# Performance work log

Hardware: AMD Instinct MI355X
Metric: run time of the kernel (lower is better)

Reference implementation:

```python
import jax, jax.numpy as jnp
import numpy as np

N = 100000   # nodes
E = 1600000  # edges (before self loops)
IN, HID, HEADS, OUT = 128, 32, 2, 32


def setup_inputs() -> dict:
    key = jax.random.key(0)
    ks = jax.random.split(key, 10)
    def glorot(k, shape, fan_in):
        return jax.random.normal(k, shape, dtype=jnp.float32) / np.sqrt(fan_in)
    return {
        "x": jax.random.normal(ks[0], (N, IN), dtype=jnp.float32),
        "edge_index": jax.random.randint(ks[1], (2, E), 0, N, dtype=jnp.int32),
        "W1": glorot(ks[2], (IN, HEADS * HID), IN),
        "a_src1": glorot(ks[3], (HEADS, HID), HID),
        "a_dst1": glorot(ks[4], (HEADS, HID), HID),
        "b1": jnp.zeros((HEADS * HID,), dtype=jnp.float32),
        "W2": glorot(ks[5], (HEADS * HID, OUT), HEADS * HID),
        "a_src2": glorot(ks[6], (1, OUT), OUT),
        "a_dst2": glorot(ks[7], (1, OUT), OUT),
        "b2": jnp.zeros((OUT,), dtype=jnp.float32),
    }


def gat_conv(x, W, a_src, a_dst, b, src, dst, n):
    """PyG-style GATConv: shared linear, edge softmax over incoming edges, sum aggregate."""
    H, C = a_src.shape
    xl = (x @ W).reshape(n, H, C)                       # [N, H, C]
    asn = jnp.einsum('nhc,hc->nh', xl, a_src)            # per-node source score
    adn = jnp.einsum('nhc,hc->nh', xl, a_dst)            # per-node dest score
    e = jax.nn.leaky_relu(asn[src] + adn[dst], 0.2)      # [E', H]
    m = jax.ops.segment_max(e, dst, num_segments=n)      # stable softmax per dest
    m = jnp.where(jnp.isfinite(m), m, 0.0)
    ex = jnp.exp(e - m[dst])
    denom = jax.ops.segment_sum(ex, dst, num_segments=n)
    alpha = ex / (denom[dst] + 1e-16)                    # [E', H]
    out = jax.ops.segment_sum(xl[src] * alpha[:, :, None], dst, num_segments=n)
    return out.reshape(n, H * C) + b


def reference(x, edge_index, W1, a_src1, a_dst1, b1, W2, a_src2, a_dst2, b2):
    n = x.shape[0]
    loop = jnp.arange(n, dtype=edge_index.dtype)         # add self loops (PyG default)
    src = jnp.concatenate([edge_index[0], loop])
    dst = jnp.concatenate([edge_index[1], loop])
    h = jax.nn.relu(gat_conv(x, W1, a_src1, a_dst1, b1, src, dst, n))
    # F.dropout(p=0.5) is identity in eval mode
    return gat_conv(h, W2, a_src2, a_dst2, b2, src, dst, n)
```

## Files before the change

### kernel.cpp

```cpp
#include <hip/hip_runtime.h>
#include <hip/hip_fp16.h>


#define BS 256
#define PCHUNK 8192
#define CAPB 5632
#define GPAD 16

typedef _Float16 half8 __attribute__((ext_vector_type(8)));
typedef float f32x4 __attribute__((ext_vector_type(4)));

__global__ __launch_bounds__(BS) void k_init(int* __restrict__ gcursor, int nbuk) {
    for (int i = threadIdx.x; i < nbuk; i += BS) gcursor[i * GPAD] = i * CAPB;
}

__global__ __launch_bounds__(BS) void k_pg1(const int* __restrict__ ei, int E, int n,
                                            int* __restrict__ gcursor, int* __restrict__ ppair,
                                            const float* __restrict__ x, const float* __restrict__ W,
                                            const float* __restrict__ asrc, const float* __restrict__ adst,
                                            __half* __restrict__ xl, float* __restrict__ sc, int gC) {
    __shared__ _Float16 smem[8192];
    int tid = threadIdx.x;
    if ((int)blockIdx.x < gC) {
        int* cnt  = (int*)smem;
        int* gpos = cnt + 512;
        int* lcur = cnt + 1024;
        cnt[tid] = 0; cnt[tid + 256] = 0;
        lcur[tid] = 0; lcur[tid + 256] = 0;
        __syncthreads();
        const int* dstp = ei + E;
        int base = blockIdx.x * PCHUNK;
        bool full = (base + PCHUNK <= E);
        if (full) {
            const int4* dv = (const int4*)(dstp + base) + tid * 8;
#pragma unroll
            for (int k = 0; k < 8; k++) {
                int4 d4 = dv[k];
                atomicAdd(&cnt[d4.x >> 8], 1);
                atomicAdd(&cnt[d4.y >> 8], 1);
                atomicAdd(&cnt[d4.z >> 8], 1);
                atomicAdd(&cnt[d4.w >> 8], 1);
            }
        } else {
            for (int i = tid; base + i < E; i += BS)
                atomicAdd(&cnt[dstp[base + i] >> 8], 1);
        }
        __syncthreads();
        for (int b = tid; b < 512; b += BS) {
            int c = cnt[b];
            if (c > 0) gpos[b] = atomicAdd(&gcursor[b * GPAD], c);
        }
        __syncthreads();
        if (full) {
            const int4* sv = (const int4*)(ei + base) + tid * 8;
            const int4* dv = (const int4*)(dstp + base) + tid * 8;
#pragma unroll 2
            for (int k = 0; k < 8; k++) {
                int4 s4 = sv[k];
                int4 d4 = dv[k];
                int d, s, b, r;
                d = d4.x; s = s4.x; b = d >> 8; r = atomicAdd(&lcur[b], 1);
                ppair[gpos[b] + r] = ((d & 255) << 17) | s;
                d = d4.y; s = s4.y; b = d >> 8; r = atomicAdd(&lcur[b], 1);
                ppair[gpos[b] + r] = ((d & 255) << 17) | s;
                d = d4.z; s = s4.z; b = d >> 8; r = atomicAdd(&lcur[b], 1);
                ppair[gpos[b] + r] = ((d & 255) << 17) | s;
                d = d4.w; s = s4.w; b = d >> 8; r = atomicAdd(&lcur[b], 1);
                ppair[gpos[b] + r] = ((d & 255) << 17) | s;
            }
        } else {
            for (int i = tid; base + i < E; i += BS) {
                int s = ei[base + i], d = dstp[base + i];
                int b = d >> 8;
                int r = atomicAdd(&lcur[b], 1);
                ppair[gpos[b] + r] = ((d & 255) << 17) | s;
            }
        }
        return;
    }
    _Float16* wf = smem;
#pragma unroll
    for (int v = 0; v < 8; v++) {
        int w = (v * 256 + tid) * 4;
        float4 ww = *(const float4*)(W + w);
        int k = w >> 6, c0 = w & 63;
        int kt = k >> 5, j = k & 7, lnh = (k >> 3) & 3;
        int nt = c0 >> 4;
        int f = kt * 4 + nt;
        int bidx = (f * 64 + lnh * 16 + (c0 & 15)) * 8 + j;
        wf[bidx]      = (_Float16)ww.x;
        wf[bidx + 8]  = (_Float16)ww.y;
        wf[bidx + 16] = (_Float16)ww.z;
        wf[bidx + 24] = (_Float16)ww.w;
    }
    __syncthreads();
    int wave = tid >> 6, lane = tid & 63;
    int nb = ((blockIdx.x - gC) * 4 + wave) * 16;
    int m = lane & 15, q = lane >> 4;
    int node_m = nb + m; if (node_m >= n) node_m = n - 1;
    half8 bf[4][4];
#pragma unroll
    for (int f = 0; f < 16; f++)
        bf[f >> 2][f & 3] = *(half8*)&wf[(f * 64 + lane) * 8];
    f32x4 acc[4] = {f32x4{0,0,0,0}, f32x4{0,0,0,0}, f32x4{0,0,0,0}, f32x4{0,0,0,0}};
#pragma unroll
    for (int kt = 0; kt < 4; kt++) {
        const float* xp = x + (size_t)node_m * 128 + kt * 32 + q * 8;
        float4 xa = *(const float4*)xp;
        float4 xb = *(const float4*)(xp + 4);
        half8 a;
        a[0] = (_Float16)xa.x; a[1] = (_Float16)xa.y; a[2] = (_Float16)xa.z; a[3] = (_Float16)xa.w;
        a[4] = (_Float16)xb.x; a[5] = (_Float16)xb.y; a[6] = (_Float16)xb.z; a[7] = (_Float16)xb.w;
#pragma unroll
        for (int nt = 0; nt < 4; nt++)
            acc[nt] = __builtin_amdgcn_mfma_f32_16x16x32_f16(a, bf[kt][nt], acc[nt], 0, 0, 0);
    }
    int c = lane & 15;
    float a_s[4], a_d[4];
#pragma unroll
    for (int nt = 0; nt < 4; nt++) { a_s[nt] = asrc[nt * 16 + c]; a_d[nt] = adst[nt * 16 + c]; }
#pragma unroll
    for (int r = 0; r < 4; r++) {
        int node = nb + q * 4 + r;
        bool ok = node < n;
        float v0 = acc[0][r], v1 = acc[1][r], v2 = acc[2][r], v3 = acc[3][r];
        float as0 = v0 * a_s[0] + v1 * a_s[1];
        float as1 = v2 * a_s[2] + v3 * a_s[3];
        float ad0 = v0 * a_d[0] + v1 * a_d[1];
        float ad1 = v2 * a_d[2] + v3 * a_d[3];
#pragma unroll
        for (int off = 1; off < 16; off <<= 1) {
            as0 += __shfl_xor(as0, off); as1 += __shfl_xor(as1, off);
            ad0 += __shfl_xor(ad0, off); ad1 += __shfl_xor(ad1, off);
        }
        if (ok) {
            __half* row = xl + (size_t)node * 64;
            row[c]      = __float2half(v0);
            row[16 + c] = __float2half(v1);
            row[32 + c] = __float2half(v2);
            row[48 + c] = __float2half(v3);
            if (c == 0) ((float4*)sc)[node] = make_float4(as0, as1, ad0, ad1);
        }
    }
}

__global__ __launch_bounds__(BS) void k_bucket(const int* __restrict__ ppair,
                                               const int* __restrict__ gcursor, int n,
                                               int* __restrict__ col,
                                               int* __restrict__ row_ptr, int* __restrict__ row_end) {
    __shared__ int ldeg[256];
    __shared__ int lscan[256];
    __shared__ int lcur[256];
    __shared__ int lcol[CAPB];
    int b = blockIdx.x;
    int t = threadIdx.x;
    int lo = b << 8;
    int hi = lo + 256; if (hi > n) hi = n;
    int W = hi - lo;
    int base = b * CAPB;
    int cnt = gcursor[b * GPAD] - base;
    if (cnt > CAPB) cnt = CAPB;
    ldeg[t] = 0;
    __syncthreads();
    for (int i = t; i < cnt; i += BS)
        atomicAdd(&ldeg[ppair[base + i] >> 17], 1);
    __syncthreads();
    lscan[t] = ldeg[t];
    __syncthreads();
    for (int off = 1; off < 256; off <<= 1) {
        int a = (t >= off) ? lscan[t - off] : 0;
        __syncthreads();
        lscan[t] += a;
        __syncthreads();
    }
    {
        int e0 = lscan[t] - ldeg[t];
        lcur[t] = e0;
        if (t < W) { row_ptr[lo + t] = base + e0; row_end[lo + t] = base + e0 + ldeg[t]; }
    }
    __syncthreads();
    for (int i = t; i < cnt; i += BS) {
        int p = ppair[base + i];
        int r = atomicAdd(&lcur[p >> 17], 1);
        if (r < CAPB) lcol[r] = p & 131071;
    }
    __syncthreads();
    for (int i = t; i < cnt; i += BS) col[base + i] = lcol[i];
}

__global__ __launch_bounds__(BS) void k_ag1g2(const int* __restrict__ row_ptr, const int* __restrict__ row_end,
                                              const int* __restrict__ col, const __half* __restrict__ xl,
                                              const float* __restrict__ sc, const float* __restrict__ asrc,
                                              const float* __restrict__ b1,
                                              const float* __restrict__ W2,
                                              const float* __restrict__ as2, const float* __restrict__ ad2,
                                              __half* __restrict__ xl2, float* __restrict__ sc2, int n) {
    __shared__ _Float16 hsh[32 * 72];
    __shared__ _Float16 wf2[2048];
    int tid = threadIdx.x;
#pragma unroll
    for (int v = 0; v < 2; v++) {
        int w = (v * 256 + tid) * 4;
        float4 ww = *(const float4*)(W2 + w);
        int k = w >> 5, c0 = w & 31;
        int kt = k >> 5, j = k & 7, lnh = (k >> 3) & 3;
        int nt = c0 >> 4;
        int f = kt * 2 + nt;
        int bidx = (f * 64 + lnh * 16 + (c0 & 15)) * 8 + j;
        wf2[bidx]      = (_Float16)ww.x;
        wf2[bidx + 8]  = (_Float16)ww.y;
        wf2[bidx + 16] = (_Float16)ww.z;
        wf2[bidx + 24] = (_Float16)ww.w;
    }
    int node_local = tid >> 3;
    int node = blockIdx.x * 32 + node_local;
    int tc = tid & 7;
    int lane = tid & 63;
    int tb = lane & 56;
    bool alive = node < n;
    int nodeC = alive ? node : n - 1;
    float4 acA = ((const float4*)asrc)[tc * 2];
    float4 acB = ((const float4*)asrc)[tc * 2 + 1];
    int s0 = row_ptr[nodeC], e1 = row_end[nodeC];
    float4 sn = ((const float4*)sc)[nodeC];
    bool hh0 = tc < 4;
    float adn = hh0 ? sn.z : sn.w;
    float es0 = sn.x + sn.z; es0 = fmaxf(es0, 0.2f * es0);
    float es1 = sn.y + sn.w; es1 = fmaxf(es1, 0.2f * es1);
    float xs = __expf(hh0 ? es0 : es1);
    uint4 rawS = *(const uint4*)(xl + (size_t)nodeC * 64 + tc * 8);
    __half2 sh0 = *(__half2*)&rawS.x, sh1 = *(__half2*)&rawS.y;
    __half2 sh2 = *(__half2*)&rawS.z, sh3 = *(__half2*)&rawS.w;
    float acc0 = xs * __low2float(sh0), acc1 = xs * __high2float(sh0);
    float acc2 = xs * __low2float(sh1), acc3 = xs * __high2float(sh1);
    float acc4 = xs * __low2float(sh2), acc5 = xs * __high2float(sh2);
    float acc6 = xs * __low2float(sh3), acc7 = xs * __high2float(sh3);
    float den = xs;
    int deg = e1 - s0;
    int mx = deg;
    mx = max(mx, __shfl_xor(mx, 8));
    mx = max(mx, __shfl_xor(mx, 16));
    mx = max(mx, __shfl_xor(mx, 32));
    int nch = (mx + 7) >> 3;
    for (int ci = 0; ci < nch; ci++) {
        int pos = s0 + ci * 8;
        int m = e1 - pos; m = m < 0 ? 0 : (m > 8 ? 8 : m);
        int srcv = (tc < m) ? col[pos + tc] : 0;
#pragma unroll
        for (int kb = 0; kb < 8; kb += 4) {
            int rem = m - kb;
            if (rem > 0) {
                int nv = rem < 4 ? rem : 4;
                uint4 rr[4];
#pragma unroll
                for (int k = 0; k < 4; k++) {
                    if (k < nv) {
                        int sE = __shfl(srcv, tb + kb + k);
                        rr[k] = *(const uint4*)(xl + (size_t)sE * 64 + tc * 8);
                    }
                }
#pragma unroll
                for (int k = 0; k < 4; k++) {
                    if (k < nv) {
                        __half2 q0 = *(__half2*)&rr[k].x, q1 = *(__half2*)&rr[k].y;
                        __half2 q2 = *(__half2*)&rr[k].z, q3 = *(__half2*)&rr[k].w;
                        float f0 = __low2float(q0), f1 = __high2float(q0);
                        float f2 = __low2float(q1), f3 = __high2float(q1);
                        float f4 = __low2float(q2), f5 = __high2float(q2);
                        float f6 = __low2float(q3), f7 = __high2float(q3);
                        float dA = f0 * acA.x + f1 * acA.y + f2 * acA.z + f3 * acA.w;
                        float dB = f4 * acB.x + f5 * acB.y + f6 * acB.z + f7 * acB.w;
                        float dot = dA + dB;
                        dot += __shfl_xor(dot, 1);
                        dot += __shfl_xor(dot, 2);
                        float e = dot + adn; e = fmaxf(e, 0.2f * e);
                        float w = __expf(e);
                        acc0 = fmaf(w, f0, acc0); acc1 = fmaf(w, f1, acc1);
                        acc2 = fmaf(w, f2, acc2); acc3 = fmaf(w, f3, acc3);
                        acc4 = fmaf(w, f4, acc4); acc5 = fmaf(w, f5, acc5);
                        acc6 = fmaf(w, f6, acc6); acc7 = fmaf(w, f7, acc7);
                        den += w;
                    }
                }
            }
        }
    }
    float dinv = 1.f / (den + 1e-16f);
    {
        float4 bvA = ((const float4*)b1)[tc * 2];
        float4 bvB = ((const float4*)b1)[tc * 2 + 1];
        __half2 p0 = __floats2half2_rn(fmaxf(fmaf(acc0, dinv, bvA.x), 0.f),
                                       fmaxf(fmaf(acc1, dinv, bvA.y), 0.f));
        __half2 p1 = __floats2half2_rn(fmaxf(fmaf(acc2, dinv, bvA.z), 0.f),
                                       fmaxf(fmaf(acc3, dinv, bvA.w), 0.f));
        __half2 p2 = __floats2half2_rn(fmaxf(fmaf(acc4, dinv, bvB.x), 0.f),
                                       fmaxf(fmaf(acc5, dinv, bvB.y), 0.f));
        __half2 p3 = __floats2half2_rn(fmaxf(fmaf(acc6, dinv, bvB.z), 0.f),
                                       fmaxf(fmaf(acc7, dinv, bvB.w), 0.f));
        uint4 o;
        o.x = *(unsigned int*)&p0; o.y = *(unsigned int*)&p1;
        o.z = *(unsigned int*)&p2; o.w = *(unsigned int*)&p3;
        *(uint4*)&hsh[node_local * 72 + tc * 8] = o;
    }
    __syncthreads();
    int wave = tid >> 6;
    if (wave < 2) {
        int m2 = lane & 15, q2 = lane >> 4;
        int nl = wave * 16 + m2;
        half8 bf[2][2];
#pragma unroll
        for (int f = 0; f < 4; f++)
            bf[f >> 1][f & 1] = *(half8*)&wf2[(f * 64 + lane) * 8];
        f32x4 acc2g[2] = {f32x4{0,0,0,0}, f32x4{0,0,0,0}};
#pragma unroll
        for (int kt = 0; kt < 2; kt++) {
            half8 a = *(half8*)&hsh[nl * 72 + kt * 32 + q2 * 8];
#pragma unroll
            for (int nt = 0; nt < 2; nt++)
                acc2g[nt] = __builtin_amdgcn_mfma_f32_16x16x32_f16(a, bf[kt][nt], acc2g[nt], 0, 0, 0);
        }
        int c = lane & 15;
        float a_s[2], a_d[2];
#pragma unroll
        for (int nt = 0; nt < 2; nt++) { a_s[nt] = as2[nt * 16 + c]; a_d[nt] = ad2[nt * 16 + c]; }
#pragma unroll
        for (int r = 0; r < 4; r++) {
            int nl_r = wave * 16 + q2 * 4 + r;
            int node_r = blockIdx.x * 32 + nl_r;
            bool ok = node_r < n;
            float v0 = acc2g[0][r], v1 = acc2g[1][r];
            float as = v0 * a_s[0] + v1 * a_s[1];
            float ad = v0 * a_d[0] + v1 * a_d[1];
#pragma unroll
            for (int off = 1; off < 16; off <<= 1) {
                as += __shfl_xor(as, off); ad += __shfl_xor(ad, off);
            }
            if (ok) {
                __half* row = xl2 + (size_t)node_r * 32;
                row[c]      = __float2half(v0);
                row[16 + c] = __float2half(v1);
                if (c == 0) ((float2*)sc2)[node_r] = make_float2(as, ad);
            }
        }
    }
}

__global__ __launch_bounds__(BS) void k_agg2(const int* __restrict__ row_ptr, const int* __restrict__ row_end,
                                             const int* __restrict__ col, const __half* __restrict__ xl,
                                             const float* __restrict__ sc, const float* __restrict__ asrc,
                                             const float* __restrict__ b2,
                                             float* __restrict__ out, int n) {
    int tid = blockIdx.x * BS + threadIdx.x;
    int node = tid >> 2;
    int tc = threadIdx.x & 3;
    int lane = threadIdx.x & 63;
    int tb = lane & 60;
    bool alive = node < n;
    if (!alive) node = n - 1;
    float4 acA = ((const float4*)asrc)[tc * 2];
    float4 acB = ((const float4*)asrc)[tc * 2 + 1];
    int s0 = row_ptr[node], e1 = row_end[node];
    float2 sn = ((const float2*)sc)[node];
    float adn = sn.y;
    float es = sn.x + adn; es = fmaxf(es, 0.2f * es);
    float xs = __expf(es);
    uint4 rawS = *(const uint4*)(xl + (size_t)node * 32 + tc * 8);
    __half2 sh0 = *(__half2*)&rawS.x, sh1 = *(__half2*)&rawS.y;
    __half2 sh2 = *(__half2*)&rawS.z, sh3 = *(__half2*)&rawS.w;
    float acc0 = xs * __low2float(sh0), acc1 = xs * __high2float(sh0);
    float acc2 = xs * __low2float(sh1), acc3 = xs * __high2float(sh1);
    float acc4 = xs * __low2float(sh2), acc5 = xs * __high2float(sh2);
    float acc6 = xs * __low2float(sh3), acc7 = xs * __high2float(sh3);
    float den = xs;
    int deg = e1 - s0;
    int mx = deg;
    mx = max(mx, __shfl_xor(mx, 4));
    mx = max(mx, __shfl_xor(mx, 8));
    mx = max(mx, __shfl_xor(mx, 16));
    mx = max(mx, __shfl_xor(mx, 32));
    int nch = (mx + 3) >> 2;
    for (int ci = 0; ci < nch; ci++) {
        int pos = s0 + ci * 4;
        int m = e1 - pos; m = m < 0 ? 0 : (m > 4 ? 4 : m);
        int srcv = (tc < m) ? col[pos + tc] : 0;
        if (m > 0) {
            uint4 rr[4];
#pragma unroll
            for (int k = 0; k < 4; k++) {
                if (k < m) {
                    int sE = __shfl(srcv, tb + k);
                    rr[k] = *(const uint4*)(xl + (size_t)sE * 32 + tc * 8);
                }
            }
#pragma unroll
            for (int k = 0; k < 4; k++) {
                if (k < m) {
                    __half2 q0 = *(__half2*)&rr[k].x, q1 = *(__half2*)&rr[k].y;
                    __half2 q2 = *(__half2*)&rr[k].z, q3 = *(__half2*)&rr[k].w;
                    float f0 = __low2float(q0), f1 = __high2float(q0);
                    float f2 = __low2float(q1), f3 = __high2float(q1);
                    float f4 = __low2float(q2), f5 = __high2float(q2);
                    float f6 = __low2float(q3), f7 = __high2float(q3);
                    float dA = f0 * acA.x + f1 * acA.y + f2 * acA.z + f3 * acA.w;
                    float dB = f4 * acB.x + f5 * acB.y + f6 * acB.z + f7 * acB.w;
                    float dot = dA + dB;
                    dot += __shfl_xor(dot, 1);
                    dot += __shfl_xor(dot, 2);
                    float e = dot + adn; e = fmaxf(e, 0.2f * e);
                    float w = __expf(e);
                    acc0 = fmaf(w, f0, acc0); acc1 = fmaf(w, f1, acc1);
                    acc2 = fmaf(w, f2, acc2); acc3 = fmaf(w, f3, acc3);
                    acc4 = fmaf(w, f4, acc4); acc5 = fmaf(w, f5, acc5);
                    acc6 = fmaf(w, f6, acc6); acc7 = fmaf(w, f7, acc7);
                    den += w;
                }
            }
        }
    }
    float dinv = 1.f / (den + 1e-16f);
    if (alive) {
        float4 bvA = ((const float4*)b2)[tc * 2];
        float4 bvB = ((const float4*)b2)[tc * 2 + 1];
        float4 oA, oB;
        oA.x = fmaf(acc0, dinv, bvA.x);
        oA.y = fmaf(acc1, dinv, bvA.y);
        oA.z = fmaf(acc2, dinv, bvA.z);
        oA.w = fmaf(acc3, dinv, bvA.w);
        oB.x = fmaf(acc4, dinv, bvB.x);
        oB.y = fmaf(acc5, dinv, bvB.y);
        oB.z = fmaf(acc6, dinv, bvB.z);
        oB.w = fmaf(acc7, dinv, bvB.w);
        float4* orow = (float4*)(out + (size_t)node * 32);
        orow[tc * 2]     = oA;
        orow[tc * 2 + 1] = oB;
    }
}

extern "C" void kernel_launch(void* const* d_in, const int* in_sizes, int n_in,
                              void* d_out, int out_size, void* d_ws, size_t ws_size,
                              hipStream_t stream) {
    const float* x    = (const float*)d_in[0];
    const int*   ei   = (const int*)d_in[1];
    const float* W1   = (const float*)d_in[2];
    const float* as1  = (const float*)d_in[3];
    const float* ad1  = (const float*)d_in[4];
    const float* b1   = (const float*)d_in[5];
    const float* W2   = (const float*)d_in[6];
    const float* as2  = (const float*)d_in[7];
    const float* ad2  = (const float*)d_in[8];
    const float* b2   = (const float*)d_in[9];
    int n = in_sizes[0] / 128;
    int E = in_sizes[1] / 2;
    int NBUK = (n + 255) >> 8;

    char* w = (char*)d_ws;
    auto alloc = [&](size_t bytes) -> char* {
        char* p = w; w += (bytes + 255) / 256 * 256; return p;
    };
    int*    gcursor = (int*)alloc((size_t)NBUK * GPAD * 4);
    int*    ppair   = (int*)alloc((size_t)NBUK * CAPB * 4);
    int*    col     = (int*)alloc((size_t)NBUK * CAPB * 4);
    int*    row_ptr = (int*)alloc((size_t)n * 4);
    int*    row_end = (int*)alloc((size_t)n * 4);
    __half* xl1     = (__half*)alloc((size_t)n * 64 * 2);
    float*  sc1     = (float*)alloc((size_t)n * 4 * 4);
    __half* xl2     = (__half*)alloc((size_t)n * 32 * 2);
    float*  sc2     = (float*)alloc((size_t)n * 2 * 4);

    int gC  = (E + PCHUNK - 1) / PCHUNK;
    int gG  = (n + 63) / 64;
    int gA1 = (n * 8 + BS - 1) / BS;
    int gA2 = (n * 4 + BS - 1) / BS;

    k_init   <<<1, BS, 0, stream>>>(gcursor, NBUK);
    k_pg1    <<<gC + gG, BS, 0, stream>>>(ei, E, n, gcursor, ppair,
                                          x, W1, as1, ad1, xl1, sc1, gC);
    k_bucket <<<NBUK, BS, 0, stream>>>(ppair, gcursor, n, col, row_ptr, row_end);
    k_ag1g2  <<<gA1, BS, 0, stream>>>(row_ptr, row_end, col, xl1, sc1, as1, b1,
                                      W2, as2, ad2, xl2, sc2, n);
    k_agg2   <<<gA2, BS, 0, stream>>>(row_ptr, row_end, col, xl2, sc2, as2, b2,
                                      (float*)d_out, n);
}
```

Measured before the change: 210.6 us.

## Quantize layer-1 features to int8 per-row and gather precomputed source scores

Layer-1 projected features are stored as int8 with a per-node scale instead of fp16, halving the bytes gathered per edge in the first aggregation. Both aggregation kernels now load the precomputed per-node source attention score through the edge list rather than recomputing it with a per-edge dot product and shuffle reduction. The node score array is split into source and destination parts. The int8 quantization adds accuracy loss and an extra scattered float4 score load per edge.

```diff
diff --git a/kernel.cpp b/kernel.cpp
--- a/kernel.cpp
+++ b/kernel.cpp
@@ -18,7 +18,8 @@
                                             int* __restrict__ gcursor, int* __restrict__ ppair,
                                             const float* __restrict__ x, const float* __restrict__ W,
                                             const float* __restrict__ asrc, const float* __restrict__ adst,
-                                            __half* __restrict__ xl, float* __restrict__ sc, int gC) {
+                                            signed char* __restrict__ xl, float* __restrict__ scA,
+                                            float* __restrict__ scD, int gC) {
     __shared__ _Float16 smem[8192];
     int tid = threadIdx.x;
     if ((int)blockIdx.x < gC) {
@@ -128,18 +129,25 @@
         float as1 = v2 * a_s[2] + v3 * a_s[3];
         float ad0 = v0 * a_d[0] + v1 * a_d[1];
         float ad1 = v2 * a_d[2] + v3 * a_d[3];
+        float mxv = fmaxf(fmaxf(fabsf(v0), fabsf(v1)), fmaxf(fabsf(v2), fabsf(v3)));
 #pragma unroll
         for (int off = 1; off < 16; off <<= 1) {
             as0 += __shfl_xor(as0, off); as1 += __shfl_xor(as1, off);
             ad0 += __shfl_xor(ad0, off); ad1 += __shfl_xor(ad1, off);
+            mxv = fmaxf(mxv, __shfl_xor(mxv, off));
         }
         if (ok) {
-            __half* row = xl + (size_t)node * 64;
-            row[c]      = __float2half(v0);
-            row[16 + c] = __float2half(v1);
-            row[32 + c] = __float2half(v2);
-            row[48 + c] = __float2half(v3);
-            if (c == 0) ((float4*)sc)[node] = make_float4(as0, as1, ad0, ad1);
+            float inv = mxv > 1e-30f ? 127.f / mxv : 0.f;
+            float scl = mxv * (1.f / 127.f);
+            signed char* row = xl + (size_t)node * 64;
+            row[c]      = (signed char)(int)rintf(v0 * inv);
+            row[16 + c] = (signed char)(int)rintf(v1 * inv);
+            row[32 + c] = (signed char)(int)rintf(v2 * inv);
+            row[48 + c] = (signed char)(int)rintf(v3 * inv);
+            if (c == 0) {
+                ((float4*)scA)[node] = make_float4(as0, as1, scl, 0.f);
+                ((float2*)scD)[node] = make_float2(ad0, ad1);
+            }
         }
     }
 }
@@ -189,8 +197,8 @@
 }
 
 __global__ __launch_bounds__(BS) void k_ag1g2(const int* __restrict__ row_ptr, const int* __restrict__ row_end,
-                                              const int* __restrict__ col, const __half* __restrict__ xl,
-                                              const float* __restrict__ sc, const float* __restrict__ asrc,
+                                              const int* __restrict__ col, const signed char* __restrict__ xl,
+                                              const float* __restrict__ scA, const float* __restrict__ scD,
                                               const float* __restrict__ b1,
                                               const float* __restrict__ W2,
                                               const float* __restrict__ as2, const float* __restrict__ ad2,
@@ -219,22 +227,25 @@
     int tb = lane & 56;
     bool alive = node < n;
     int nodeC = alive ? node : n - 1;
-    float4 acA = ((const float4*)asrc)[tc * 2];
-    float4 acB = ((const float4*)asrc)[tc * 2 + 1];
     int s0 = row_ptr[nodeC], e1 = row_end[nodeC];
-    float4 sn = ((const float4*)sc)[nodeC];
+    float4 sA = ((const float4*)scA)[nodeC];
+    float2 sD = ((const float2*)scD)[nodeC];
     bool hh0 = tc < 4;
-    float adn = hh0 ? sn.z : sn.w;
-    float es0 = sn.x + sn.z; es0 = fmaxf(es0, 0.2f * es0);
-    float es1 = sn.y + sn.w; es1 = fmaxf(es1, 0.2f * es1);
+    float adn = hh0 ? sD.x : sD.y;
+    float es0 = sA.x + sD.x; es0 = fmaxf(es0, 0.2f * es0);
+    float es1 = sA.y + sD.y; es1 = fmaxf(es1, 0.2f * es1);
     float xs = __expf(hh0 ? es0 : es1);
-    uint4 rawS = *(const uint4*)(xl + (size_t)nodeC * 64 + tc * 8);
-    __half2 sh0 = *(__half2*)&rawS.x, sh1 = *(__half2*)&rawS.y;
-    __half2 sh2 = *(__half2*)&rawS.z, sh3 = *(__half2*)&rawS.w;
-    float acc0 = xs * __low2float(sh0), acc1 = xs * __high2float(sh0);
-    float acc2 = xs * __low2float(sh1), acc3 = xs * __high2float(sh1);
-    float acc4 = xs * __low2float(sh2), acc5 = xs * __high2float(sh2);
-    float acc6 = xs * __low2float(sh3), acc7 = xs * __high2float(sh3);
+    uint2 rawS = *(const uint2*)(xl + (size_t)nodeC * 64 + tc * 8);
+    float ws0 = xs * sA.z;
+    int sx = (int)rawS.x, sy = (int)rawS.y;
+    float acc0 = ws0 * (float)(signed char)(sx);
+    float acc1 = ws0 * (float)(signed char)(sx >> 8);
+    float acc2 = ws0 * (float)(signed char)(sx >> 16);
+    float acc3 = ws0 * (float)(signed char)(sx >> 24);
+    float acc4 = ws0 * (float)(signed char)(sy);
+    float acc5 = ws0 * (float)(signed char)(sy >> 8);
+    float acc6 = ws0 * (float)(signed char)(sy >> 16);
+    float acc7 = ws0 * (float)(signed char)(sy >> 24);
     float den = xs;
     int deg = e1 - s0;
     int mx = deg;
@@ -245,40 +256,44 @@
     for (int ci = 0; ci < nch; ci++) {
         int pos = s0 + ci * 8;
         int m = e1 - pos; m = m < 0 ? 0 : (m > 8 ? 8 : m);
-        int srcv = (tc < m) ? col[pos + tc] : 0;
+        int srcv = 0; float sgx = 0.f, sgy = 0.f, sgz = 0.f;
+        if (tc < m) {
+            srcv = col[pos + tc];
+            float4 sg = ((const float4*)scA)[srcv];
+            sgx = sg.x; sgy = sg.y; sgz = sg.z;
+        }
 #pragma unroll
         for (int kb = 0; kb < 8; kb += 4) {
             int rem = m - kb;
             if (rem > 0) {
                 int nv = rem < 4 ? rem : 4;
-                uint4 rr[4];
+                uint2 rr[4];
 #pragma unroll
                 for (int k = 0; k < 4; k++) {
                     if (k < nv) {
                         int sE = __shfl(srcv, tb + kb + k);
-                        rr[k] = *(const uint4*)(xl + (size_t)sE * 64 + tc * 8);
+                        rr[k] = *(const uint2*)(xl + (size_t)sE * 64 + tc * 8);
                     }
                 }
 #pragma unroll
                 for (int k = 0; k < 4; k++) {
                     if (k < nv) {
-                        __half2 q0 = *(__half2*)&rr[k].x, q1 = *(__half2*)&rr[k].y;
-                        __half2 q2 = *(__half2*)&rr[k].z, q3 = *(__half2*)&rr[k].w;
-                        float f0 = __low2float(q0), f1 = __high2float(q0);
-                        float f2 = __low2float(q1), f3 = __high2float(q1);
-                        float f4 = __low2float(q2), f5 = __high2float(q2);
-                        float f6 = __low2float(q3), f7 = __high2float(q3);
-                        float dA = f0 * acA.x + f1 * acA.y + f2 * acA.z + f3 * acA.w;
-                        float dB = f4 * acB.x + f5 * acB.y + f6 * acB.z + f7 * acB.w;
-                        float dot = dA + dB;
-                        dot += __shfl_xor(dot, 1);
-                        dot += __shfl_xor(dot, 2);
-                        float e = dot + adn; e = fmaxf(e, 0.2f * e);
+                        float a0 = __shfl(sgx, tb + kb + k);
+                        float a1 = __shfl(sgy, tb + kb + k);
+                        float sc_ = __shfl(sgz, tb + kb + k);
+                        float as_ = hh0 ? a0 : a1;
+                        float e = as_ + adn; e = fmaxf(e, 0.2f * e);
                         float w = __expf(e);
-                        acc0 = fmaf(w, f0, acc0); acc1 = fmaf(w, f1, acc1);
-                        acc2 = fmaf(w, f2, acc2); acc3 = fmaf(w, f3, acc3);
-                        acc4 = fmaf(w, f4, acc4); acc5 = fmaf(w, f5, acc5);
-                        acc6 = fmaf(w, f6, acc6); acc7 = fmaf(w, f7, acc7);
+                        float wq = w * sc_;
+                        int wx = (int)rr[k].x, wy = (int)rr[k].y;
+                        acc0 = fmaf(wq, (float)(signed char)(wx), acc0);
+                        acc1 = fmaf(wq, (float)(signed char)(wx >> 8), acc1);
+                        acc2 = fmaf(wq, (float)(signed char)(wx >> 16), acc2);
+                        acc3 = fmaf(wq, (float)(signed char)(wx >> 24), acc3);
+                        acc4 = fmaf(wq, (float)(signed char)(wy), acc4);
+                        acc5 = fmaf(wq, (float)(signed char)(wy >> 8), acc5);
+                        acc6 = fmaf(wq, (float)(signed char)(wy >> 16), acc6);
+                        acc7 = fmaf(wq, (float)(signed char)(wy >> 24), acc7);
                         den += w;
                     }
                 }
@@ -357,8 +372,6 @@
     int tb = lane & 60;
     bool alive = node < n;
     if (!alive) node = n - 1;
-    float4 acA = ((const float4*)asrc)[tc * 2];
-    float4 acB = ((const float4*)asrc)[tc * 2 + 1];
     int s0 = row_ptr[node], e1 = row_end[node];
     float2 sn = ((const float2*)sc)[node];
     float adn = sn.y;
@@ -382,7 +395,11 @@
     for (int ci = 0; ci < nch; ci++) {
         int pos = s0 + ci * 4;
         int m = e1 - pos; m = m < 0 ? 0 : (m > 4 ? 4 : m);
-        int srcv = (tc < m) ? col[pos + tc] : 0;
+        int srcv = 0; float sA = 0.f;
+        if (tc < m) {
+            srcv = col[pos + tc];
+            sA = sc[(size_t)srcv * 2];
+        }
         if (m > 0) {
             uint4 rr[4];
 #pragma unroll
@@ -395,23 +412,15 @@
 #pragma unroll
             for (int k = 0; k < 4; k++) {
                 if (k < m) {
+                    float s = __shfl(sA, tb + k);
+                    float e = s + adn; e = fmaxf(e, 0.2f * e);
+                    float w = __expf(e);
                     __half2 q0 = *(__half2*)&rr[k].x, q1 = *(__half2*)&rr[k].y;
                     __half2 q2 = *(__half2*)&rr[k].z, q3 = *(__half2*)&rr[k].w;
-                    float f0 = __low2float(q0), f1 = __high2float(q0);
-                    float f2 = __low2float(q1), f3 = __high2float(q1);
-                    float f4 = __low2float(q2), f5 = __high2float(q2);
-                    float f6 = __low2float(q3), f7 = __high2float(q3);
-                    float dA = f0 * acA.x + f1 * acA.y + f2 * acA.z + f3 * acA.w;
-                    float dB = f4 * acB.x + f5 * acB.y + f6 * acB.z + f7 * acB.w;
-                    float dot = dA + dB;
-                    dot += __shfl_xor(dot, 1);
-                    dot += __shfl_xor(dot, 2);
-                    float e = dot + adn; e = fmaxf(e, 0.2f * e);
-                    float w = __expf(e);
-                    acc0 = fmaf(w, f0, acc0); acc1 = fmaf(w, f1, acc1);
-                    acc2 = fmaf(w, f2, acc2); acc3 = fmaf(w, f3, acc3);
-                    acc4 = fmaf(w, f4, acc4); acc5 = fmaf(w, f5, acc5);
-                    acc6 = fmaf(w, f6, acc6); acc7 = fmaf(w, f7, acc7);
+                    acc0 = fmaf(w, __low2float(q0), acc0); acc1 = fmaf(w, __high2float(q0), acc1);
+                    acc2 = fmaf(w, __low2float(q1), acc2); acc3 = fmaf(w, __high2float(q1), acc3);
+                    acc4 = fmaf(w, __low2float(q2), acc4); acc5 = fmaf(w, __high2float(q2), acc5);
+                    acc6 = fmaf(w, __low2float(q3), acc6); acc7 = fmaf(w, __high2float(q3), acc7);
                     den += w;
                 }
             }
@@ -462,8 +471,9 @@
     int*    col     = (int*)alloc((size_t)NBUK * CAPB * 4);
     int*    row_ptr = (int*)alloc((size_t)n * 4);
     int*    row_end = (int*)alloc((size_t)n * 4);
-    __half* xl1     = (__half*)alloc((size_t)n * 64 * 2);
-    float*  sc1     = (float*)alloc((size_t)n * 4 * 4);
+    signed char* xl1 = (signed char*)alloc((size_t)n * 64);
+    float*  scA     = (float*)alloc((size_t)n * 4 * 4);
+    float*  scD     = (float*)alloc((size_t)n * 2 * 4);
     __half* xl2     = (__half*)alloc((size_t)n * 32 * 2);
     float*  sc2     = (float*)alloc((size_t)n * 2 * 4);
 
@@ -474,9 +484,9 @@
 
     k_init   <<<1, BS, 0, stream>>>(gcursor, NBUK);
     k_pg1    <<<gC + gG, BS, 0, stream>>>(ei, E, n, gcursor, ppair,
-                                          x, W1, as1, ad1, xl1, sc1, gC);
+                                          x, W1, as1, ad1, xl1, scA, scD, gC);
     k_bucket <<<NBUK, BS, 0, stream>>>(ppair, gcursor, n, col, row_ptr, row_end);
-    k_ag1g2  <<<gA1, BS, 0, stream>>>(row_ptr, row_end, col, xl1, sc1, as1, b1,
+    k_ag1g2  <<<gA1, BS, 0, stream>>>(row_ptr, row_end, col, xl1, scA, scD, b1,
                                       W2, as2, ad2, xl2, sc2, n);
     k_agg2   <<<gA2, BS, 0, stream>>>(row_ptr, row_end, col, xl2, sc2, as2, b2,
                                       (float*)d_out, n);
```

After: 211.3 us. No clear change (+0.3%).
